# Performance work log

Hardware: AMD Instinct MI355X
Metric: run time of the kernel (lower is better)

Reference implementation:

```python
import jax, jax.numpy as jnp
import numpy as np

N_NODES = 20000
N_EDGES = 320000
IN_CH = 512
HEADS = 4
OUT_CH = 128
NEG_SLOPE = 0.2  # PyG GATConv default leaky_relu slope


def setup_inputs() -> dict:
    key = jax.random.key(0)
    k1, k2, k3, k4, k5 = jax.random.split(key, 5)
    x = jax.random.normal(k1, (N_NODES, IN_CH), dtype=jnp.float32)
    edge_index = jax.random.randint(k2, (2, N_EDGES), 0, N_NODES, dtype=jnp.int64)
    # Learned parameters (glorot-ish scaling)
    W = jax.random.normal(k3, (IN_CH, HEADS * OUT_CH), dtype=jnp.float32) * np.float32(1.0 / np.sqrt(IN_CH))
    att_src = jax.random.normal(k4, (HEADS, OUT_CH), dtype=jnp.float32) * np.float32(0.1)
    att_dst = jax.random.normal(k5, (HEADS, OUT_CH), dtype=jnp.float32) * np.float32(0.1)
    bias = jnp.zeros((OUT_CH,), dtype=jnp.float32)
    return {"x": x, "W": W, "att_src": att_src, "att_dst": att_dst, "bias": bias, "edge_index": edge_index}


def reference(x, W, att_src, att_dst, bias, edge_index):
    N = x.shape[0]
    H, C = att_src.shape
    # add self-loops (PyG GATConv default add_self_loops=True)
    loop = jnp.arange(N, dtype=edge_index.dtype)
    ei = jnp.concatenate([edge_index, jnp.stack([loop, loop])], axis=1)
    src, dst = ei[0], ei[1]
    # linear projection: [N, H, C]
    xl = (x @ W).reshape(N, H, C)
    # per-node attention halves: [N, H]
    a_s = jnp.einsum('nhc,hc->nh', xl, att_src)
    a_d = jnp.einsum('nhc,hc->nh', xl, att_dst)
    # per-edge logits + segment softmax over incoming edges (grouped by dst)
    alpha = jax.nn.leaky_relu(a_s[src] + a_d[dst], negative_slope=NEG_SLOPE)  # [E, H]
    amax = jax.ops.segment_max(alpha, dst, num_segments=N)  # every node has a self-loop -> no empty segments
    ae = jnp.exp(alpha - amax[dst])
    denom = jax.ops.segment_sum(ae, dst, num_segments=N)
    alpha = ae / (denom[dst] + 1e-16)
    # weighted scatter-add of source features: [N, H, C]
    out = jax.ops.segment_sum(alpha[:, :, None] * xl[src], dst, num_segments=N)
    # concat=False -> mean over heads, then bias [C]
    out = out.mean(axis=1) + bias
    return jax.nn.elu(out)
```

## Files before the change

kernel.cpp:

```cpp
#include <hip/hip_runtime.h>
#include <math.h>

#define N_NODES 20000
#define N_PAD 20096
#define N_EDGES 320000
#define IN_CH 512
#define HEADS 4
#define OUT_CH 128
#define HC 512
#define NEG_SLOPE 0.2f

#define CVX_BLOCKS 5024
#define CVW_BLOCKS 64
#define CNT_BLOCKS 1250

#define GEMM_WGS 1256

typedef __attribute__((ext_vector_type(8))) short short8;
typedef __attribute__((ext_vector_type(4))) float float4v;

__device__ __forceinline__ int detect_is64(const int* __restrict__ ei32) {
    int is64 = 1;
    #pragma unroll
    for (int i = 0; i < 32; i++) is64 &= (ei32[2 * i + 1] == 0);
    return is64;
}

__device__ __forceinline__ int edge_at(const void* ei, int is64, long long idx) {
    return is64 ? (int)((const long long*)ei)[idx] : ((const int*)ei)[idx];
}

__device__ __forceinline__ unsigned short f2bf(float f) {
    union { float f; unsigned u; } v; v.f = f;
    unsigned r = v.u + 0x7fffu + ((v.u >> 16) & 1u);
    return (unsigned short)(r >> 16);
}

__device__ __forceinline__ void bf8_decode(uint4 r, float* f) {
    f[0] = __uint_as_float(r.x << 16); f[1] = __uint_as_float(r.x & 0xffff0000u);
    f[2] = __uint_as_float(r.y << 16); f[3] = __uint_as_float(r.y & 0xffff0000u);
    f[4] = __uint_as_float(r.z << 16); f[5] = __uint_as_float(r.z & 0xffff0000u);
    f[6] = __uint_as_float(r.w << 16); f[7] = __uint_as_float(r.w & 0xffff0000u);
}

__device__ __forceinline__ float leaky(float t) { return t > 0.f ? t : NEG_SLOPE * t; }

__device__ __forceinline__ float sel_head(float4 w, int hd) {
    float lo = (hd & 1) ? w.y : w.x;
    float hi = (hd & 1) ? w.w : w.z;
    return (hd & 2) ? hi : lo;
}

__global__ __launch_bounds__(256) void fusedA_kernel(const float* __restrict__ x,
                                                     const float* __restrict__ W,
                                                     unsigned short* __restrict__ xb,
                                                     unsigned short* __restrict__ Wt,
                                                     const void* __restrict__ ei,
                                                     int* __restrict__ counts,
                                                     int* __restrict__ epos) {
    __shared__ float tile[64][65];
    int b = blockIdx.x;
    if (b < CVX_BLOCKS) {
        size_t i = ((size_t)b * 256 + threadIdx.x) * 8;
        unsigned short o[8];
        if (i < (size_t)N_NODES * IN_CH) {
            float4 f0 = *(const float4*)&x[i];
            float4 f1 = *(const float4*)&x[i + 4];
            o[0] = f2bf(f0.x); o[1] = f2bf(f0.y); o[2] = f2bf(f0.z); o[3] = f2bf(f0.w);
            o[4] = f2bf(f1.x); o[5] = f2bf(f1.y); o[6] = f2bf(f1.z); o[7] = f2bf(f1.w);
        } else {
            for (int k = 0; k < 8; k++) o[k] = 0;
        }
        *(short8*)&xb[i] = *(short8*)o;
    } else if (b < CVX_BLOCKS + CVW_BLOCKS) {
        int idx = b - CVX_BLOCKS;
        int k0 = (idx & 7) * 64, n0 = (idx >> 3) * 64;
        int t = threadIdx.x, r = t >> 6, c = t & 63;
        for (int rr = r; rr < 64; rr += 4)
            tile[rr][c] = W[(size_t)(k0 + rr) * HC + n0 + c];
        __syncthreads();
        for (int rr = r; rr < 64; rr += 4)
            Wt[(size_t)(n0 + rr) * IN_CH + k0 + c] = f2bf(tile[c][rr]);
    } else {
        int is64 = detect_is64((const int*)ei);
        int e = (b - CVX_BLOCKS - CVW_BLOCKS) * 256 + threadIdx.x;
        if (e < N_EDGES) {
            int dst = edge_at(ei, is64, (long long)N_EDGES + e);
            int p = atomicAdd(&counts[dst], 1);
            epos[e] = p;
        }
    }
}

__global__ __launch_bounds__(256) void gemm_kernel(const unsigned short* __restrict__ A,
                                                   const unsigned short* __restrict__ Bt,
                                                   unsigned short* __restrict__ Cb,
                                                   const float* __restrict__ att_s,
                                                   const float* __restrict__ att_d,
                                                   float* __restrict__ a_s,
                                                   float* __restrict__ a_d) {
    __shared__ __align__(16) unsigned short As[3][64 * 32];
    __shared__ __align__(16) unsigned short Bs[3][128 * 32];
    __shared__ float ssum[64][2];
    __shared__ float dsum[64][2];

    const int bid = blockIdx.x;
    const int w = (bid & 7) * 157 + (bid >> 3);
    const int bm = (w >> 2) * 64;
    const int bn = (w & 3) * 128;

    const int t = threadIdx.x;
    const int wv = t >> 6, lane = t & 63;
    const int wm = wv & 1, wn = wv >> 1;
    const int lm = lane & 15, lk = lane >> 4;

    float4v acc[2][4];
    #pragma unroll
    for (int i = 0; i < 2; i++)
        #pragma unroll
        for (int j = 0; j < 4; j++) acc[i][j] = (float4v){0.f, 0.f, 0.f, 0.f};

    const int srow = t >> 2;
    const int sk   = ((t & 3) ^ ((t >> 3) & 3)) * 8;
    const int swr  = (lk ^ ((lm >> 1) & 3)) * 8;

#define GEMM_STAGE(buf, kof)                                                                   \
    {                                                                                          \
        const unsigned short* gA = A + (size_t)(bm + srow) * IN_CH + (kof) + sk;               \
        __builtin_amdgcn_global_load_lds((const __attribute__((address_space(1))) void*)gA,    \
            (__attribute__((address_space(3))) void*)&As[buf][t * 8], 16, 0, 0);               \
        _Pragma("unroll")                                                                      \
        for (int q = 0; q < 2; q++) {                                                          \
            const unsigned short* gB = Bt + (size_t)(bn + q * 64 + srow) * IN_CH + (kof) + sk; \
            __builtin_amdgcn_global_load_lds((const __attribute__((address_space(1))) void*)gB,\
                (__attribute__((address_space(3))) void*)&Bs[buf][q * 2048 + t * 8], 16, 0, 0);\
        }                                                                                      \
    }

    GEMM_STAGE(0, 0);
    GEMM_STAGE(1, 32);
    #pragma unroll
    for (int kk = 0; kk < 16; ++kk) {
        const int cur = kk % 3;
        if (kk < 14) {
            GEMM_STAGE((kk + 2) % 3, (kk + 2) * 32);
            asm volatile("s_waitcnt vmcnt(6)" ::: "memory");
        } else if (kk == 14) {
            asm volatile("s_waitcnt vmcnt(3)" ::: "memory");
        } else {
            asm volatile("s_waitcnt vmcnt(0)" ::: "memory");
        }
        __builtin_amdgcn_s_barrier();
        __builtin_amdgcn_sched_barrier(0);

        short8 af[2], bf[4];
        #pragma unroll
        for (int i = 0; i < 2; i++)
            af[i] = *(const short8*)&As[cur][(wm * 32 + i * 16 + lm) * 32 + swr];
        #pragma unroll
        for (int j = 0; j < 4; j++)
            bf[j] = *(const short8*)&Bs[cur][(wn * 64 + j * 16 + lm) * 32 + swr];
        #pragma unroll
        for (int i = 0; i < 2; i++)
            #pragma unroll
            for (int j = 0; j < 4; j++)
                acc[i][j] = __builtin_amdgcn_mfma_f32_16x16x32_bf16(af[i], bf[j], acc[i][j], 0, 0, 0);

        __builtin_amdgcn_sched_barrier(0);
        __builtin_amdgcn_s_barrier();
    }
#undef GEMM_STAGE

    #pragma unroll
    for (int i = 0; i < 2; i++) {
        #pragma unroll
        for (int r = 0; r < 4; r++) {
            int row = bm + wm * 32 + i * 16 + lk * 4 + r;
            if (row < N_NODES) {
                #pragma unroll
                for (int j = 0; j < 4; j++) {
                    int col = bn + wn * 64 + j * 16 + lm;
                    Cb[(size_t)row * HC + col] = f2bf(acc[i][j][r]);
                }
            }
        }
    }

    const int h = bn >> 7;
    float as_w[4], ad_w[4];
    #pragma unroll
    for (int j = 0; j < 4; j++) {
        int col = bn + wn * 64 + j * 16 + lm;
        as_w[j] = att_s[col];
        ad_w[j] = att_d[col];
    }
    float ps[2][4], pd[2][4];
    #pragma unroll
    for (int i = 0; i < 2; i++)
        #pragma unroll
        for (int r = 0; r < 4; r++) {
            float s = 0.f, d = 0.f;
            #pragma unroll
            for (int j = 0; j < 4; j++) { s += acc[i][j][r] * as_w[j]; d += acc[i][j][r] * ad_w[j]; }
            ps[i][r] = s; pd[i][r] = d;
        }
    #pragma unroll
    for (int off = 1; off < 16; off <<= 1) {
        #pragma unroll
        for (int i = 0; i < 2; i++)
            #pragma unroll
            for (int r = 0; r < 4; r++) {
                ps[i][r] += __shfl_xor(ps[i][r], off, 64);
                pd[i][r] += __shfl_xor(pd[i][r], off, 64);
            }
    }
    if (lm == 0) {
        #pragma unroll
        for (int i = 0; i < 2; i++)
            #pragma unroll
            for (int r = 0; r < 4; r++) {
                int rl = wm * 32 + i * 16 + lk * 4 + r;
                ssum[rl][wn] = ps[i][r];
                dsum[rl][wn] = pd[i][r];
            }
    }
    __syncthreads();
    if (t < 64) {
        int row = bm + t;
        if (row < N_NODES) {
            a_s[row * 4 + h] = ssum[t][0] + ssum[t][1];
            a_d[row * 4 + h] = dsum[t][0] + dsum[t][1];
        }
    }
}

__global__ __launch_bounds__(1024) void scan_kernel(const int* __restrict__ counts,
                                                    int* __restrict__ offsets) {
    const int CHUNK = 20;
    int tid = threadIdx.x;
    int base = tid * CHUNK;
    int c[CHUNK];
    #pragma unroll
    for (int k = 0; k < CHUNK; k++) {
        int i = base + k;
        c[k] = (i < N_NODES) ? counts[i] : 0;
    }
    int pre[CHUNK];
    int sum = 0;
    #pragma unroll
    for (int k = 0; k < CHUNK; k++) { pre[k] = sum; sum += c[k]; }

    int lane = tid & 63, wvv = tid >> 6;
    int s = sum;
    #pragma unroll
    for (int off = 1; off < 64; off <<= 1) {
        int u = __shfl_up(s, off, 64);
        if (lane >= off) s += u;
    }
    __shared__ int wsum[16];
    if (lane == 63) wsum[wvv] = s;
    __syncthreads();
    if (tid < 16) {
        int u = wsum[tid];
        #pragma unroll
        for (int off = 1; off < 16; off <<= 1) {
            int w = __shfl_up(u, off, 64);
            if (tid >= off) u += w;
        }
        wsum[tid] = u;
    }
    __syncthreads();
    int wbase = (wvv == 0) ? 0 : wsum[wvv - 1];
    int excl = wbase + s - sum;
    #pragma unroll
    for (int k = 0; k < CHUNK; k++) {
        int i = base + k;
        if (i < N_NODES) offsets[i] = excl + pre[k];
    }
    if (tid == 1023) offsets[N_NODES] = wbase + s;
}

__global__ __launch_bounds__(256) void scatterw_kernel(const void* __restrict__ ei,
                                                       const int* __restrict__ offsets,
                                                       const int* __restrict__ epos,
                                                       int* __restrict__ sorted_src,
                                                       const float* __restrict__ a_s,
                                                       const float* __restrict__ a_d,
                                                       float* __restrict__ edge_w) {
    int is64 = detect_is64((const int*)ei);
    int e = blockIdx.x * 256 + threadIdx.x;
    if (e < N_EDGES) {
        int dst = edge_at(ei, is64, (long long)N_EDGES + e);
        int src = edge_at(ei, is64, e);
        int pos = offsets[dst] + epos[e];
        sorted_src[pos] = src;
        float4 as4 = *(const float4*)&a_s[src * 4];
        float4 ad4 = *(const float4*)&a_d[dst * 4];
        float4 w;
        w.x = __expf(leaky(as4.x + ad4.x));
        w.y = __expf(leaky(as4.y + ad4.y));
        w.z = __expf(leaky(as4.z + ad4.z));
        w.w = __expf(leaky(as4.w + ad4.w));
        *(float4*)&edge_w[(size_t)pos * 4] = w;
    }
}

__global__ __launch_bounds__(256) void gather_kernel(const unsigned short* __restrict__ xlb,
                                                     const float* __restrict__ a_s,
                                                     const float* __restrict__ a_d,
                                                     const int* __restrict__ offsets,
                                                     const int* __restrict__ sorted_src,
                                                     const float* __restrict__ edge_w,
                                                     const float* __restrict__ bias,
                                                     float* __restrict__ out) {
    __shared__ float cl[2][64][9];
    int wv = threadIdx.x >> 6;
    int nib = wv >> 1;
    int sub = wv & 1;
    int node = blockIdx.x * 2 + nib;
    int lane = threadIdx.x & 63;
    int hd = lane >> 4;
    int beg = offsets[node], end = offsets[node + 1];

    const unsigned short* xrow = xlb + lane * 8;
    float acc[8] = {0, 0, 0, 0, 0, 0, 0, 0};
    float denom = 0.f;

    int c0 = beg + sub * 4;
    int s0 = 0, s1 = 0, s2 = 0, s3 = 0;
    float w0 = 0.f, w1 = 0.f, w2 = 0.f, w3 = 0.f;
    if (c0 < end) {
        int lim = end - 1;
        int i1 = c0 + 1 > lim ? lim : c0 + 1;
        int i2 = c0 + 2 > lim ? lim : c0 + 2;
        int i3 = c0 + 3 > lim ? lim : c0 + 3;
        s0 = sorted_src[c0]; s1 = sorted_src[i1]; s2 = sorted_src[i2]; s3 = sorted_src[i3];
        float4 t0 = *(const float4*)&edge_w[(size_t)c0 * 4];
        float4 t1 = *(const float4*)&edge_w[(size_t)i1 * 4];
        float4 t2 = *(const float4*)&edge_w[(size_t)i2 * 4];
        float4 t3 = *(const float4*)&edge_w[(size_t)i3 * 4];
        w0 = sel_head(t0, hd);
        w1 = (c0 + 1 < end) ? sel_head(t1, hd) : 0.f;
        w2 = (c0 + 2 < end) ? sel_head(t2, hd) : 0.f;
        w3 = (c0 + 3 < end) ? sel_head(t3, hd) : 0.f;
    }

    if (sub == 0) {
        float4 as4 = *(const float4*)&a_s[node * 4];
        float4 ad4 = *(const float4*)&a_d[node * 4];
        float4 ws;
        ws.x = __expf(leaky(as4.x + ad4.x));
        ws.y = __expf(leaky(as4.y + ad4.y));
        ws.z = __expf(leaky(as4.z + ad4.z));
        ws.w = __expf(leaky(as4.w + ad4.w));
        float w = sel_head(ws, hd);
        denom = w;
        uint4 r = *(const uint4*)(xrow + (size_t)node * HC);
        float f[8];
        bf8_decode(r, f);
        #pragma unroll
        for (int k = 0; k < 8; k++) acc[k] = w * f[k];
    }

    for (; c0 < end; c0 += 8) {
        uint4 r0 = *(const uint4*)(xrow + (size_t)s0 * HC);
        uint4 r1 = *(const uint4*)(xrow + (size_t)s1 * HC);
        uint4 r2 = *(const uint4*)(xrow + (size_t)s2 * HC);
        uint4 r3 = *(const uint4*)(xrow + (size_t)s3 * HC);

        int c1 = c0 + 8;
        int n0 = 0, n1 = 0, n2 = 0, n3 = 0;
        float v0 = 0.f, v1 = 0.f, v2 = 0.f, v3 = 0.f;
        if (c1 < end) {
            int lim = end - 1;
            int i1 = c1 + 1 > lim ? lim : c1 + 1;
            int i2 = c1 + 2 > lim ? lim : c1 + 2;
            int i3 = c1 + 3 > lim ? lim : c1 + 3;
            n0 = sorted_src[c1]; n1 = sorted_src[i1]; n2 = sorted_src[i2]; n3 = sorted_src[i3];
            float4 t0 = *(const float4*)&edge_w[(size_t)c1 * 4];
            float4 t1 = *(const float4*)&edge_w[(size_t)i1 * 4];
            float4 t2 = *(const float4*)&edge_w[(size_t)i2 * 4];
            float4 t3 = *(const float4*)&edge_w[(size_t)i3 * 4];
            v0 = sel_head(t0, hd);
            v1 = (c1 + 1 < end) ? sel_head(t1, hd) : 0.f;
            v2 = (c1 + 2 < end) ? sel_head(t2, hd) : 0.f;
            v3 = (c1 + 3 < end) ? sel_head(t3, hd) : 0.f;
        }

        denom += (w0 + w1) + (w2 + w3);
        float f0[8], f1[8], f2[8], f3[8];
        bf8_decode(r0, f0);
        bf8_decode(r1, f1);
        bf8_decode(r2, f2);
        bf8_decode(r3, f3);
        #pragma unroll
        for (int k = 0; k < 8; k++)
            acc[k] += (w0 * f0[k] + w1 * f1[k]) + (w2 * f2[k] + w3 * f3[k]);

        s0 = n0; s1 = n1; s2 = n2; s3 = n3;
        w0 = v0; w1 = v1; w2 = v2; w3 = v3;
    }

    if (sub == 1) {
        #pragma unroll
        for (int k = 0; k < 8; k++) cl[nib][lane][k] = acc[k];
        cl[nib][lane][8] = denom;
    }
    __syncthreads();
    if (sub == 0) {
        #pragma unroll
        for (int k = 0; k < 8; k++) acc[k] += cl[nib][lane][k];
        denom += cl[nib][lane][8];

        float rd = 0.25f / (denom + 1e-16f);
        float v[8];
        #pragma unroll
        for (int k = 0; k < 8; k++) {
            float t = acc[k] * rd;
            t += __shfl_xor(t, 16, 64);
            t += __shfl_xor(t, 32, 64);
            v[k] = t;
        }
        if (hd == 0) {
            float4 b0 = *(const float4*)&bias[lane * 8];
            float4 b1 = *(const float4*)&bias[lane * 8 + 4];
            float o[8];
            o[0] = v[0] + b0.x; o[1] = v[1] + b0.y; o[2] = v[2] + b0.z; o[3] = v[3] + b0.w;
            o[4] = v[4] + b1.x; o[5] = v[5] + b1.y; o[6] = v[6] + b1.z; o[7] = v[7] + b1.w;
            #pragma unroll
            for (int k = 0; k < 8; k++) o[k] = o[k] > 0.f ? o[k] : expm1f(o[k]);
            *(float4*)&out[(size_t)node * OUT_CH + lane * 8]     = make_float4(o[0], o[1], o[2], o[3]);
            *(float4*)&out[(size_t)node * OUT_CH + lane * 8 + 4] = make_float4(o[4], o[5], o[6], o[7]);
        }
    }
}

extern "C" void kernel_launch(void* const* d_in, const int* in_sizes, int n_in,
                              void* d_out, int out_size, void* d_ws, size_t ws_size,
                              hipStream_t stream) {
    const float* x       = (const float*)d_in[0];
    const float* W       = (const float*)d_in[1];
    const float* att_src = (const float*)d_in[2];
    const float* att_dst = (const float*)d_in[3];
    const float* bias    = (const float*)d_in[4];
    const void*  ei      = d_in[5];
    float* out = (float*)d_out;

    char* ws = (char*)d_ws;
    size_t off = 0;
    unsigned short* xlb = (unsigned short*)(ws + off); off += (size_t)N_PAD * HC * sizeof(unsigned short);
    float* a_s     = (float*)(ws + off); off += (size_t)N_NODES * HEADS * sizeof(float);
    float* a_d     = (float*)(ws + off); off += (size_t)N_NODES * HEADS * sizeof(float);
    int* counts    = (int*)(ws + off);   off += (size_t)N_NODES * sizeof(int);
    int* offsets   = (int*)(ws + off);   off += (size_t)(N_NODES + 1) * sizeof(int);
    off = (off + 15) & ~(size_t)15;
    int* epos      = (int*)(ws + off);   off += (size_t)N_EDGES * sizeof(int);
    int* sorted_src = (int*)(ws + off);  off += (size_t)N_EDGES * sizeof(int);
    off = (off + 15) & ~(size_t)15;
    float* edge_w  = (float*)(ws + off); off += (size_t)N_EDGES * HEADS * sizeof(float);
    unsigned short* xb = (unsigned short*)(ws + off); off += (size_t)N_PAD * IN_CH * sizeof(unsigned short);
    unsigned short* Wt = (unsigned short*)(ws + off); off += (size_t)IN_CH * HC * sizeof(unsigned short);

    hipMemsetAsync(counts, 0, N_NODES * sizeof(int), stream);
    fusedA_kernel<<<CVX_BLOCKS + CVW_BLOCKS + CNT_BLOCKS, 256, 0, stream>>>(x, W, xb, Wt, ei, counts, epos);
    gemm_kernel<<<GEMM_WGS, 256, 0, stream>>>(xb, Wt, xlb, att_src, att_dst, a_s, a_d);
    scan_kernel<<<1, 1024, 0, stream>>>(counts, offsets);
    scatterw_kernel<<<(N_EDGES + 255) / 256, 256, 0, stream>>>(ei, offsets, epos, sorted_src, a_s, a_d, edge_w);
    gather_kernel<<<N_NODES / 2, 256, 0, stream>>>(xlb, a_s, a_d, offsets, sorted_src, edge_w, bias, out);
}
```

Measured before the change: 209.7 us.

## Widen GEMM tile to 64x256 with double buffering and per-wave head reductions

Each GEMM workgroup now computes a 64x256 output tile instead of 64x128, halving the workgroup count and re-reading each A tile half as often. The LDS pipeline drops from triple to double buffering to fit the larger B tile, and launch bounds request 3 blocks per SM. Because each wave now owns one full head, the attention dot products are written directly without the shared-memory cross-wave reduction. The XCD-aware block remapping is adjusted for the new grid. The cost is more accumulator registers per thread and less prefetch depth for hiding load latency.

```diff
diff --git a/kernel.cpp b/kernel.cpp
--- a/kernel.cpp
+++ b/kernel.cpp
@@ -14,7 +14,9 @@
 #define CVW_BLOCKS 64
 #define CNT_BLOCKS 1250
 
-#define GEMM_WGS 1256
+#define GEMM_WGS 628
+#define GEMM_XQ 78
+#define GEMM_XR 4
 
 typedef __attribute__((ext_vector_type(8))) short short8;
 typedef __attribute__((ext_vector_type(4))) float float4v;
@@ -92,33 +94,33 @@
     }
 }
 
-__global__ __launch_bounds__(256) void gemm_kernel(const unsigned short* __restrict__ A,
-                                                   const unsigned short* __restrict__ Bt,
-                                                   unsigned short* __restrict__ Cb,
-                                                   const float* __restrict__ att_s,
-                                                   const float* __restrict__ att_d,
-                                                   float* __restrict__ a_s,
-                                                   float* __restrict__ a_d) {
-    __shared__ __align__(16) unsigned short As[3][64 * 32];
-    __shared__ __align__(16) unsigned short Bs[3][128 * 32];
-    __shared__ float ssum[64][2];
-    __shared__ float dsum[64][2];
+__global__ __launch_bounds__(256, 3) void gemm_kernel(const unsigned short* __restrict__ A,
+                                                      const unsigned short* __restrict__ Bt,
+                                                      unsigned short* __restrict__ Cb,
+                                                      const float* __restrict__ att_s,
+                                                      const float* __restrict__ att_d,
+                                                      float* __restrict__ a_s,
+                                                      float* __restrict__ a_d) {
+    __shared__ __align__(16) unsigned short As[2][64 * 32];
+    __shared__ __align__(16) unsigned short Bs[2][256 * 32];
 
     const int bid = blockIdx.x;
-    const int w = (bid & 7) * 157 + (bid >> 3);
-    const int bm = (w >> 2) * 64;
-    const int bn = (w & 3) * 128;
+    const int xcd = bid & 7, rank = bid >> 3;
+    const int w = (xcd < GEMM_XR) ? xcd * (GEMM_XQ + 1) + rank
+                                  : GEMM_XR * (GEMM_XQ + 1) + (xcd - GEMM_XR) * GEMM_XQ + rank;
+    const int bm = (w >> 1) * 64;
+    const int bn = (w & 1) * 256;
 
     const int t = threadIdx.x;
     const int wv = t >> 6, lane = t & 63;
     const int wm = wv & 1, wn = wv >> 1;
     const int lm = lane & 15, lk = lane >> 4;
 
-    float4v acc[2][4];
+    float4v acc[2][8];
     #pragma unroll
     for (int i = 0; i < 2; i++)
         #pragma unroll
-        for (int j = 0; j < 4; j++) acc[i][j] = (float4v){0.f, 0.f, 0.f, 0.f};
+        for (int j = 0; j < 8; j++) acc[i][j] = (float4v){0.f, 0.f, 0.f, 0.f};
 
     const int srow = t >> 2;
     const int sk   = ((t & 3) ^ ((t >> 3) & 3)) * 8;
@@ -130,7 +132,7 @@
         __builtin_amdgcn_global_load_lds((const __attribute__((address_space(1))) void*)gA,    \
             (__attribute__((address_space(3))) void*)&As[buf][t * 8], 16, 0, 0);               \
         _Pragma("unroll")                                                                      \
-        for (int q = 0; q < 2; q++) {                                                          \
+        for (int q = 0; q < 4; q++) {                                                          \
             const unsigned short* gB = Bt + (size_t)(bn + q * 64 + srow) * IN_CH + (kof) + sk; \
             __builtin_amdgcn_global_load_lds((const __attribute__((address_space(1))) void*)gB,\
                 (__attribute__((address_space(3))) void*)&Bs[buf][q * 2048 + t * 8], 16, 0, 0);\
@@ -138,32 +140,29 @@
     }
 
     GEMM_STAGE(0, 0);
-    GEMM_STAGE(1, 32);
     #pragma unroll
     for (int kk = 0; kk < 16; ++kk) {
-        const int cur = kk % 3;
-        if (kk < 14) {
-            GEMM_STAGE((kk + 2) % 3, (kk + 2) * 32);
-            asm volatile("s_waitcnt vmcnt(6)" ::: "memory");
-        } else if (kk == 14) {
-            asm volatile("s_waitcnt vmcnt(3)" ::: "memory");
+        const int cur = kk & 1;
+        if (kk < 15) {
+            GEMM_STAGE(cur ^ 1, (kk + 1) * 32);
+            asm volatile("s_waitcnt vmcnt(5)" ::: "memory");
         } else {
             asm volatile("s_waitcnt vmcnt(0)" ::: "memory");
         }
         __builtin_amdgcn_s_barrier();
         __builtin_amdgcn_sched_barrier(0);
 
-        short8 af[2], bf[4];
+        short8 af[2], bf[8];
         #pragma unroll
         for (int i = 0; i < 2; i++)
             af[i] = *(const short8*)&As[cur][(wm * 32 + i * 16 + lm) * 32 + swr];
         #pragma unroll
-        for (int j = 0; j < 4; j++)
-            bf[j] = *(const short8*)&Bs[cur][(wn * 64 + j * 16 + lm) * 32 + swr];
+        for (int j = 0; j < 8; j++)
+            bf[j] = *(const short8*)&Bs[cur][(wn * 128 + j * 16 + lm) * 32 + swr];
         #pragma unroll
         for (int i = 0; i < 2; i++)
             #pragma unroll
-            for (int j = 0; j < 4; j++)
+            for (int j = 0; j < 8; j++)
                 acc[i][j] = __builtin_amdgcn_mfma_f32_16x16x32_bf16(af[i], bf[j], acc[i][j], 0, 0, 0);
 
         __builtin_amdgcn_sched_barrier(0);
@@ -178,19 +177,19 @@
             int row = bm + wm * 32 + i * 16 + lk * 4 + r;
             if (row < N_NODES) {
                 #pragma unroll
-                for (int j = 0; j < 4; j++) {
-                    int col = bn + wn * 64 + j * 16 + lm;
+                for (int j = 0; j < 8; j++) {
+                    int col = bn + wn * 128 + j * 16 + lm;
                     Cb[(size_t)row * HC + col] = f2bf(acc[i][j][r]);
                 }
             }
         }
     }
 
-    const int h = bn >> 7;
-    float as_w[4], ad_w[4];
-    #pragma unroll
-    for (int j = 0; j < 4; j++) {
-        int col = bn + wn * 64 + j * 16 + lm;
+    const int h = (bn >> 7) + wn;
+    float as_w[8], ad_w[8];
+    #pragma unroll
+    for (int j = 0; j < 8; j++) {
+        int col = h * 128 + j * 16 + lm;
         as_w[j] = att_s[col];
         ad_w[j] = att_d[col];
     }
@@ -201,7 +200,7 @@
         for (int r = 0; r < 4; r++) {
             float s = 0.f, d = 0.f;
             #pragma unroll
-            for (int j = 0; j < 4; j++) { s += acc[i][j][r] * as_w[j]; d += acc[i][j][r] * ad_w[j]; }
+            for (int j = 0; j < 8; j++) { s += acc[i][j][r] * as_w[j]; d += acc[i][j][r] * ad_w[j]; }
             ps[i][r] = s; pd[i][r] = d;
         }
     #pragma unroll
@@ -219,18 +218,12 @@
         for (int i = 0; i < 2; i++)
             #pragma unroll
             for (int r = 0; r < 4; r++) {
-                int rl = wm * 32 + i * 16 + lk * 4 + r;
-                ssum[rl][wn] = ps[i][r];
-                dsum[rl][wn] = pd[i][r];
+                int row = bm + wm * 32 + i * 16 + lk * 4 + r;
+                if (row < N_NODES) {
+                    a_s[row * 4 + h] = ps[i][r];
+                    a_d[row * 4 + h] = pd[i][r];
+                }
             }
-    }
-    __syncthreads();
-    if (t < 64) {
-        int row = bm + t;
-        if (row < N_NODES) {
-            a_s[row * 4 + h] = ssum[t][0] + ssum[t][1];
-            a_d[row * 4 + h] = dsum[t][0] + dsum[t][1];
-        }
     }
 }
 
```

Measured after the change: 208.6 us. Within noise of the previous version (-0.6%).
